# Kernel optimization log

Hardware: AMD Instinct MI355X
Metric: run time of the kernel (lower is better)

Reference implementation:

```python
import jax, jax.numpy as jnp
import numpy as np

N = 50000      # nodes per graph
E = 1_600_000  # edges per graph (before self-loops)
D = 128        # node feature dim
H = 9          # attention heads
C = 8          # channels per head
HC = H * C     # 72
NEG_SLOPE = 0.2


def setup_inputs() -> dict:
    key = jax.random.key(0)
    ks = iter(jax.random.split(key, 32))
    inp = {}
    for i in (1, 2, 3):
        inp[f"x{i}"] = jax.random.normal(next(ks), (N, D), dtype=jnp.float32)
        inp[f"edge_index{i}"] = jax.random.randint(next(ks), (2, E), 0, N, dtype=jnp.int64)
        inp[f"W{i}"] = jax.random.normal(next(ks), (D, HC), dtype=jnp.float32) * (1.0 / np.sqrt(D))
        inp[f"att_src{i}"] = jax.random.normal(next(ks), (H, C), dtype=jnp.float32) * 0.1
        inp[f"att_dst{i}"] = jax.random.normal(next(ks), (H, C), dtype=jnp.float32) * 0.1
        inp[f"b{i}"] = jnp.zeros((HC,), dtype=jnp.float32)
    inp["fnn_W"] = jax.random.normal(next(ks), (3 * HC, 2), dtype=jnp.float32) * (1.0 / np.sqrt(3 * HC))
    inp["fnn_b"] = jnp.zeros((2,), dtype=jnp.float32)
    return inp


def gat_conv(x, edge_index, W, att_src, att_dst, bias):
    """PyG GATConv (eval mode): linear -> per-edge LeakyReLU score -> edge softmax
    over incoming edges per dst node -> scatter-add aggregate. Self-loops added."""
    n = x.shape[0]
    loop = jnp.arange(n, dtype=edge_index.dtype)
    src = jnp.concatenate([edge_index[0], loop])  # [E+N]
    dst = jnp.concatenate([edge_index[1], loop])
    h = (x @ W).reshape(n, H, C)                  # [N,H,C]
    a_s = jnp.einsum('nhc,hc->nh', h, att_src)    # [N,H]
    a_d = jnp.einsum('nhc,hc->nh', h, att_dst)
    alpha = jax.nn.leaky_relu(a_s[src] + a_d[dst], NEG_SLOPE)   # [E+N,H]
    m = jax.ops.segment_max(alpha, dst, num_segments=n)         # stable softmax per dst
    alpha = jnp.exp(alpha - m[dst])
    denom = jax.ops.segment_sum(alpha, dst, num_segments=n)
    alpha = alpha / (denom[dst] + 1e-16)
    out = jax.ops.segment_sum(h[src] * alpha[:, :, None], dst, num_segments=n)
    return out.reshape(n, HC) + bias


def reference(x1, x2, x3, edge_index1, edge_index2, edge_index3,
              W1, att_src1, att_dst1, b1,
              W2, att_src2, att_dst2, b2,
              W3, att_src3, att_dst3, b3,
              fnn_W, fnn_b):
    o1 = gat_conv(x1, edge_index1, W1, att_src1, att_dst1, b1)
    o2 = gat_conv(x2, edge_index2, W2, att_src2, att_dst2, b2)
    o3 = gat_conv(x3, edge_index3, W3, att_src3, att_dst3, b3)
    x = jax.nn.relu(jnp.concatenate([o1, o2, o3], axis=1))  # [N, 216]
    logits = x @ fnn_W + fnn_b                              # [N, 2]
    return jax.nn.softmax(logits, axis=1)
```

## Files before the change

### kernel.cpp

```cpp
#include <hip/hip_runtime.h>
#include <hip/hip_fp16.h>

#define NN 50000
#define NE 1600000
#define DD 128
#define NH 9
#define NC 8
#define HCH 72
#define NEG 0.2f
#define NBUCK 196
#define NSEG 16
#define SPAD 17
#define EPB 16
#define BCH (256*EPB)
#define BSTRIDE 10240
#define BCSTRIDE 16
#define GEMMB2 ((NN + 63) / 64)
#define BINB ((NE + BCH - 1) / BCH)
#define AGGB ((NN * NH + 255) / 256)
#define CLP 88

typedef _Float16 f16x8 __attribute__((ext_vector_type(8)));
typedef float f32x4 __attribute__((ext_vector_type(4)));

__device__ __forceinline__ unsigned short f2h(float f) {
  return __half_as_ushort(__float2half_rn(f));
}
__device__ __forceinline__ float h2f(unsigned short u) {
  return __half2float(__ushort_as_half(u));
}
__device__ __forceinline__ float hlo(unsigned u) {
  return __half2float(__ushort_as_half((unsigned short)(u & 0xFFFFu)));
}
__device__ __forceinline__ float hhi(unsigned u) {
  return __half2float(__ushort_as_half((unsigned short)(u >> 16)));
}

struct GP {
  const float* x; const int* ei; const float* W;
  const float* as; const float* ad; const float* b;
  uint4* h2;
  unsigned short* as2;
  float* a_d; float* out;
  _Float16* wf;
  int* offs2;
  int* bcursor;
  unsigned int* pairs;
  int* csr;
};
struct GT { GP g[3]; };

__device__ __forceinline__ void accum(unsigned short u, uint4 v, float ad_n,
                                      float& denom, float4& acc0, float4& acc1) {
  float tt = h2f(u) + ad_n;
  tt = (tt > 0.f) ? tt : NEG * tt;
  const float w = __expf(tt);
  denom += w;
  acc0.x = fmaf(w, hlo(v.x), acc0.x); acc0.y = fmaf(w, hhi(v.x), acc0.y);
  acc0.z = fmaf(w, hlo(v.y), acc0.z); acc0.w = fmaf(w, hhi(v.y), acc0.w);
  acc1.x = fmaf(w, hlo(v.z), acc1.x); acc1.y = fmaf(w, hhi(v.z), acc1.y);
  acc1.z = fmaf(w, hlo(v.w), acc1.z); acc1.w = fmaf(w, hhi(v.w), acc1.w);
}

__global__ __launch_bounds__(256) void k_wpack(GT t) {
  const GP G = t.g[blockIdx.z];
  const int tid = threadIdx.x;
  for (int idx = tid; idx < 4 * 5 * 64 * 8; idx += 256) {
    const int j = idx & 7;
    const int lane = (idx >> 3) & 63;
    const int ctks = idx >> 9;
    const int ct = ctks % 5;
    const int ks = ctks / 5;
    const int k = ks * 32 + ((lane >> 4) << 3) + j;
    const int col = ct * 16 + (lane & 15);
    const float v = (col < HCH) ? G.W[k * HCH + col] : 0.f;
    G.wf[idx] = (_Float16)v;
  }
}

__global__ __launch_bounds__(256) void k_fat(GT t) {
  const GP G = t.g[blockIdx.z];
  __shared__ __align__(16) char smem[23072];
  const int tid = threadIdx.x;

  if (blockIdx.x < BINB) {
    unsigned* stage = (unsigned*)smem;
    unsigned char* bkt = (unsigned char*)(smem + 16384);
    int* hist   = (int*)(smem + 20480);
    int* gdelta = (int*)(smem + 21264);
    int* ssum   = (int*)(smem + 22048);
    const int e0 = blockIdx.x * BCH;

    for (int i = tid; i < NBUCK; i += 256) hist[i] = 0;
    __syncthreads();
    int dsts[EPB], srcs[EPB];
    #pragma unroll
    for (int k = 0; k < EPB; ++k) {
      const int e = e0 + k * 256 + tid;
      if (e < NE) {
        dsts[k] = G.ei[NE + e];
        srcs[k] = G.ei[e];
        atomicAdd(&hist[dsts[k] >> 8], 1);
      } else dsts[k] = -1;
    }
    __syncthreads();
    const int cnt_t = (tid < NBUCK) ? hist[tid] : 0;
    ssum[tid] = cnt_t;
    __syncthreads();
    int run = cnt_t;
    for (int off = 1; off < 256; off <<= 1) {
      int u = (tid >= off) ? ssum[tid - off] : 0;
      __syncthreads();
      run += u;
      ssum[tid] = run;
      __syncthreads();
    }
    const int excl = run - cnt_t;
    if (tid < NBUCK) {
      const int gbase = cnt_t ? atomicAdd(&G.bcursor[tid * BCSTRIDE], cnt_t) : 0;
      gdelta[tid] = tid * BSTRIDE + gbase - excl;
      hist[tid] = excl;
    }
    __syncthreads();
    #pragma unroll
    for (int k = 0; k < EPB; ++k) {
      if (dsts[k] >= 0) {
        const int b = dsts[k] >> 8;
        const int pos = atomicAdd(&hist[b], 1);
        stage[pos] = (unsigned)srcs[k] | ((unsigned)(dsts[k] & 255) << 16);
        bkt[pos] = (unsigned char)b;
      }
    }
    __syncthreads();
    const int total = (e0 + BCH <= NE) ? BCH : (NE - e0);
    for (int i = tid; i < total; i += 256) {
      const int b = bkt[i];
      const int addr = gdelta[b] + i;
      if (addr - b * BSTRIDE < BSTRIDE)
        G.pairs[addr] = stage[i];
    }
    return;
  }

  _Float16* Cl = (_Float16*)smem;
  const int wv = tid >> 6;
  const int ln = tid & 63;
  const int rl = ln & 15;
  const int kg = ln >> 4;
  const int n0 = (blockIdx.x - BINB) << 6;
  int arow = n0 + wv * 16 + rl;
  if (arow >= NN) arow = NN - 1;
  const float4* xr = (const float4*)(G.x + (size_t)arow * DD) + (kg << 1);
  const f16x8* wfp = (const f16x8*)G.wf;

  f32x4 acc[5];
  #pragma unroll
  for (int ct = 0; ct < 5; ++ct) acc[ct] = (f32x4){0.f, 0.f, 0.f, 0.f};

  #pragma unroll
  for (int ks = 0; ks < 4; ++ks) {
    const float4 xa = xr[ks * 8];
    const float4 xb = xr[ks * 8 + 1];
    float xs[8] = {xa.x, xa.y, xa.z, xa.w, xb.x, xb.y, xb.z, xb.w};
    f16x8 ahi, alo;
    #pragma unroll
    for (int j = 0; j < 8; ++j) {
      const _Float16 h = (_Float16)xs[j];
      ahi[j] = h;
      alo[j] = (_Float16)(xs[j] - (float)h);
    }
    #pragma unroll
    for (int ct = 0; ct < 5; ++ct) {
      const f16x8 bf = wfp[(ks * 5 + ct) * 64 + ln];
      acc[ct] = __builtin_amdgcn_mfma_f32_16x16x32_f16(ahi, bf, acc[ct], 0, 0, 0);
      acc[ct] = __builtin_amdgcn_mfma_f32_16x16x32_f16(alo, bf, acc[ct], 0, 0, 0);
    }
  }

  #pragma unroll
  for (int ct = 0; ct < 5; ++ct) {
    #pragma unroll
    for (int j = 0; j < 4; ++j)
      Cl[(wv * 16 + kg * 4 + j) * CLP + ct * 16 + rl] = (_Float16)acc[ct][j];
  }
  __syncthreads();

  for (int p = tid; p < 64 * NH; p += 256) {
    const int node = p / NH;
    const int hd = p - node * NH;
    const int n = n0 + node;
    if (n >= NN) continue;
    const uint4 hv = *(const uint4*)&Cl[node * CLP + hd * NC];
    const float h0 = hlo(hv.x), h1 = hhi(hv.x), h2v = hlo(hv.y), h3 = hhi(hv.y);
    const float h4 = hlo(hv.z), h5 = hhi(hv.z), h6 = hlo(hv.w), h7 = hhi(hv.w);
    const float4 As0 = *(const float4*)(G.as + hd * NC);
    const float4 As1 = *(const float4*)(G.as + hd * NC + 4);
    const float4 Ad0 = *(const float4*)(G.ad + hd * NC);
    const float4 Ad1 = *(const float4*)(G.ad + hd * NC + 4);
    const float ssrc = h0 * As0.x + h1 * As0.y + h2v * As0.z + h3 * As0.w
                     + h4 * As1.x + h5 * As1.y + h6 * As1.z + h7 * As1.w;
    const float sdst = h0 * Ad0.x + h1 * Ad0.y + h2v * Ad0.z + h3 * Ad0.w
                     + h4 * Ad1.x + h5 * Ad1.y + h6 * Ad1.z + h7 * Ad1.w;
    G.h2[(size_t)n * NH + hd] = hv;
    G.as2[n * NH + hd] = f2h(ssrc);
    G.a_d[n * NH + hd] = sdst;
  }
}

__global__ __launch_bounds__(256) void k_scat2(GT t) {
  const GP G = t.g[blockIdx.z];
  const int b = blockIdx.x;
  const int d0 = b << 8;
  __shared__ int cnt[256 * SPAD];
  __shared__ int ssum[256];
  __shared__ unsigned short stage[BSTRIDE];
  const int tid = threadIdx.x;
  const int estart = b * BSTRIDE;
  const int count0 = G.bcursor[b * BCSTRIDE];
  const int count = (count0 < BSTRIDE) ? count0 : BSTRIDE;
  const int eend = estart + count;
  for (int i = tid; i < 256 * SPAD; i += 256) cnt[i] = 0;
  __syncthreads();
  for (int e = estart + tid; e < eend; e += 256) {
    unsigned p = G.pairs[e];
    int key = (int)((p >> 16) * SPAD + ((p & 0xFFFFu) >> 12));
    atomicAdd(&cnt[key], 1);
  }
  __syncthreads();
  int local[NSEG];
  int sum = 0;
  #pragma unroll
  for (int i = 0; i < NSEG; ++i) { local[i] = sum; sum += cnt[tid * SPAD + i]; }
  ssum[tid] = sum;
  __syncthreads();
  int run = sum;
  for (int off = 1; off < 256; off <<= 1) {
    int u = (tid >= off) ? ssum[tid - off] : 0;
    __syncthreads();
    run += u;
    ssum[tid] = run;
    __syncthreads();
  }
  const int texcl = run - sum;
  int* o2 = G.offs2 + ((size_t)d0 << 4);
  #pragma unroll
  for (int i = 0; i < NSEG; ++i) {
    const int v = texcl + local[i];
    cnt[tid * SPAD + i] = v;
    o2[tid * NSEG + i] = estart + v;
  }
  __syncthreads();
  for (int e = estart + tid; e < eend; e += 256) {
    unsigned p = G.pairs[e];
    int key = (int)((p >> 16) * SPAD + ((p & 0xFFFFu) >> 12));
    int lpos = atomicAdd(&cnt[key], 1);
    if (lpos < BSTRIDE)
      stage[lpos] = (unsigned short)(p & 0xFFFFu);
  }
  __syncthreads();
  for (int i = tid; i < count; i += 256)
    G.csr[estart + i] = (int)stage[i];
}

__global__ __launch_bounds__(256) void k_agg(GT t) {
  const int g = blockIdx.x / AGGB;
  const GP G = t.g[g];
  const int gid = (blockIdx.x - g * AGGB) * 256 + threadIdx.x;
  const bool active = (gid < NN * NH);
  int n = 0, head = 0;
  if (active) { n = gid / NH; head = gid - n * NH; }
  float denom = 0.f;
  float4 acc0 = make_float4(0.f, 0.f, 0.f, 0.f);
  float4 acc1 = make_float4(0.f, 0.f, 0.f, 0.f);
  float ad_n = 0.f;
  int gb[5] = {0, 0, 0, 0, 0};
  if (active) {
    ad_n = G.a_d[n * NH + head];
    const int* o2 = G.offs2 + ((size_t)n << 4);
    gb[0] = o2[0]; gb[1] = o2[4]; gb[2] = o2[8]; gb[3] = o2[12]; gb[4] = o2[13];
    float sl = h2f(G.as2[n * NH + head]) + ad_n;
    sl = (sl > 0.f) ? sl : NEG * sl;
    float wl = __expf(sl);
    uint4 hs = G.h2[(size_t)n * NH + head];
    denom = wl;
    acc0.x = wl * hlo(hs.x); acc0.y = wl * hhi(hs.x);
    acc0.z = wl * hlo(hs.y); acc0.w = wl * hhi(hs.y);
    acc1.x = wl * hlo(hs.z); acc1.y = wl * hhi(hs.z);
    acc1.z = wl * hlo(hs.w); acc1.w = wl * hhi(hs.w);
  }
  #pragma unroll
  for (int sgrp = 0; sgrp < 4; ++sgrp) {
    int e = gb[sgrp];
    const int en = gb[sgrp + 1];
    for (; e + 8 <= en; e += 8) {
      const int s0 = G.csr[e];
      const int s1 = G.csr[e + 1];
      const int s2 = G.csr[e + 2];
      const int s3 = G.csr[e + 3];
      const int s4 = G.csr[e + 4];
      const int s5 = G.csr[e + 5];
      const int s6 = G.csr[e + 6];
      const int s7 = G.csr[e + 7];
      const unsigned short u0 = G.as2[s0 * NH + head];
      const unsigned short u1 = G.as2[s1 * NH + head];
      const unsigned short u2 = G.as2[s2 * NH + head];
      const unsigned short u3 = G.as2[s3 * NH + head];
      const unsigned short u4 = G.as2[s4 * NH + head];
      const unsigned short u5 = G.as2[s5 * NH + head];
      const unsigned short u6 = G.as2[s6 * NH + head];
      const unsigned short u7 = G.as2[s7 * NH + head];
      const uint4 v0 = G.h2[(size_t)s0 * NH + head];
      const uint4 v1 = G.h2[(size_t)s1 * NH + head];
      const uint4 v2 = G.h2[(size_t)s2 * NH + head];
      const uint4 v3 = G.h2[(size_t)s3 * NH + head];
      const uint4 v4 = G.h2[(size_t)s4 * NH + head];
      const uint4 v5 = G.h2[(size_t)s5 * NH + head];
      const uint4 v6 = G.h2[(size_t)s6 * NH + head];
      const uint4 v7 = G.h2[(size_t)s7 * NH + head];
      accum(u0, v0, ad_n, denom, acc0, acc1);
      accum(u1, v1, ad_n, denom, acc0, acc1);
      accum(u2, v2, ad_n, denom, acc0, acc1);
      accum(u3, v3, ad_n, denom, acc0, acc1);
      accum(u4, v4, ad_n, denom, acc0, acc1);
      accum(u5, v5, ad_n, denom, acc0, acc1);
      accum(u6, v6, ad_n, denom, acc0, acc1);
      accum(u7, v7, ad_n, denom, acc0, acc1);
    }
    if (e + 4 <= en) {
      const int s0 = G.csr[e];
      const int s1 = G.csr[e + 1];
      const int s2 = G.csr[e + 2];
      const int s3 = G.csr[e + 3];
      const unsigned short u0 = G.as2[s0 * NH + head];
      const unsigned short u1 = G.as2[s1 * NH + head];
      const unsigned short u2 = G.as2[s2 * NH + head];
      const unsigned short u3 = G.as2[s3 * NH + head];
      const uint4 v0 = G.h2[(size_t)s0 * NH + head];
      const uint4 v1 = G.h2[(size_t)s1 * NH + head];
      const uint4 v2 = G.h2[(size_t)s2 * NH + head];
      const uint4 v3 = G.h2[(size_t)s3 * NH + head];
      accum(u0, v0, ad_n, denom, acc0, acc1);
      accum(u1, v1, ad_n, denom, acc0, acc1);
      accum(u2, v2, ad_n, denom, acc0, acc1);
      accum(u3, v3, ad_n, denom, acc0, acc1);
      e += 4;
    }
    for (; e < en; ++e) {
      const int src = G.csr[e];
      const unsigned short u = G.as2[src * NH + head];
      const uint4 hv = G.h2[(size_t)src * NH + head];
      accum(u, hv, ad_n, denom, acc0, acc1);
    }
    __builtin_amdgcn_s_barrier();
  }
  if (!active) return;
  float inv = 1.f / (denom + 1e-16f);
  const float* bp = G.b + head * NC;
  float4 o0, o1;
  o0.x = acc0.x * inv + bp[0]; o0.y = acc0.y * inv + bp[1];
  o0.z = acc0.z * inv + bp[2]; o0.w = acc0.w * inv + bp[3];
  o1.x = acc1.x * inv + bp[4]; o1.y = acc1.y * inv + bp[5];
  o1.z = acc1.z * inv + bp[6]; o1.w = acc1.w * inv + bp[7];
  float4* op = (float4*)(G.out + (size_t)n * HCH + head * NC);
  op[0] = o0; op[1] = o1;
}

__global__ __launch_bounds__(256) void k_fnn(const float* __restrict__ o1,
                                             const float* __restrict__ o2,
                                             const float* __restrict__ o3,
                                             const float* __restrict__ fw,
                                             const float* __restrict__ fb,
                                             float* __restrict__ out) {
  const int tid = blockIdx.x * 256 + threadIdx.x;
  const int n = tid >> 6;
  const int lane = tid & 63;
  if (n >= NN) return;
  float acc0 = 0.f, acc1 = 0.f;
  for (int j = lane; j < 3 * HCH; j += 64) {
    const int g = j / HCH;
    const int c = j - g * HCH;
    const float* og = (g == 0) ? o1 : (g == 1) ? o2 : o3;
    float v = og[(size_t)n * HCH + c];
    v = v > 0.f ? v : 0.f;
    acc0 = fmaf(v, fw[2 * j], acc0);
    acc1 = fmaf(v, fw[2 * j + 1], acc1);
  }
  #pragma unroll
  for (int off = 32; off > 0; off >>= 1) {
    acc0 += __shfl_down(acc0, off, 64);
    acc1 += __shfl_down(acc1, off, 64);
  }
  if (lane == 0) {
    float l0 = acc0 + fb[0], l1 = acc1 + fb[1];
    float m = fmaxf(l0, l1);
    float e0 = __expf(l0 - m), e1 = __expf(l1 - m);
    float inv = 1.f / (e0 + e1);
    out[(size_t)n * 2] = e0 * inv;
    out[(size_t)n * 2 + 1] = e1 * inv;
  }
}

extern "C" void kernel_launch(void* const* d_in, const int* in_sizes, int n_in,
                              void* d_out, int out_size, void* d_ws, size_t ws_size,
                              hipStream_t stream) {
  (void)in_sizes; (void)n_in; (void)out_size; (void)ws_size;
  GT t;
  char* w = (char*)d_ws;
  size_t off = 0;
  auto carve = [&](size_t bytes) -> void* {
    void* p = w + off;
    off = (off + bytes + 255) & ~(size_t)255;
    return p;
  };
  int* bc_all = (int*)carve(3 * NBUCK * BCSTRIDE * 4);
  for (int g = 0; g < 3; ++g) {
    GP& G = t.g[g];
    G.x  = (const float*)d_in[6 * g + 0];
    G.ei = (const int*)d_in[6 * g + 1];
    G.W  = (const float*)d_in[6 * g + 2];
    G.as = (const float*)d_in[6 * g + 3];
    G.ad = (const float*)d_in[6 * g + 4];
    G.b  = (const float*)d_in[6 * g + 5];
    G.bcursor = bc_all + g * NBUCK * BCSTRIDE;
    G.h2   = (uint4*)carve((size_t)NN * NH * 16);
    G.as2  = (unsigned short*)carve((size_t)NN * NH * 2);
    G.a_d  = (float*)carve((size_t)NN * NH * 4);
    G.out  = (float*)carve((size_t)NN * HCH * 4);
    G.wf   = (_Float16*)carve((size_t)4 * 5 * 64 * 8 * 2);
    G.offs2 = (int*)carve((size_t)NBUCK * 256 * NSEG * 4);
    G.pairs = (unsigned int*)carve((size_t)NBUCK * BSTRIDE * 4);
    G.csr   = (int*)carve((size_t)NBUCK * BSTRIDE * 4);
  }
  const float* fw = (const float*)d_in[18];
  const float* fb = (const float*)d_in[19];
  float* outp = (float*)d_out;

  dim3 b256(256, 1, 1);
  hipMemsetAsync(bc_all, 0, 3 * NBUCK * BCSTRIDE * 4, stream);
  k_wpack <<<dim3(1, 1, 3), b256, 0, stream>>>(t);
  k_fat   <<<dim3(BINB + GEMMB2, 1, 3), b256, 0, stream>>>(t);
  k_scat2 <<<dim3(NBUCK, 1, 3), b256, 0, stream>>>(t);
  k_agg   <<<dim3(AGGB * 3, 1, 1), b256, 0, stream>>>(t);
  k_fnn   <<<(NN * 64 + 255) / 256, b256, 0, stream>>>(t.g[0].out, t.g[1].out, t.g[2].out, fw, fb, outp);
}
```

Measured before the change: 406.4 us.

## Recompute source attention score from gathered features instead of loading as2

Drops the precomputed fp16 per-node source score array. The aggregation kernel now recomputes the dot product of the gathered h row with att_src for each edge, which removes one scattered 2-byte gather per edge at the cost of 8 extra FMAs. The bucket-cursor memset is folded into the weight-pack kernel, saving a separate memset launch. The edge loop unroll drops from 8 to 4 and the per-group barrier becomes __syncthreads. Risks include more ALU work per edge and less memory-level parallelism from the smaller unroll.

Result: faster. 386.1 us (-5.0%).

```diff
diff --git a/kernel.cpp b/kernel.cpp
--- a/kernel.cpp
+++ b/kernel.cpp
@@ -40,7 +40,6 @@
   const float* x; const int* ei; const float* W;
   const float* as; const float* ad; const float* b;
   uint4* h2;
-  unsigned short* as2;
   float* a_d; float* out;
   _Float16* wf;
   int* offs2;
@@ -50,21 +49,27 @@
 };
 struct GT { GP g[3]; };
 
-__device__ __forceinline__ void accum(unsigned short u, uint4 v, float ad_n,
-                                      float& denom, float4& acc0, float4& acc1) {
-  float tt = h2f(u) + ad_n;
+__device__ __forceinline__ void accum2(uint4 v, const float4 As0, const float4 As1,
+                                       float ad_n, float& denom,
+                                       float4& acc0, float4& acc1) {
+  const float h0 = hlo(v.x), h1 = hhi(v.x), h2v = hlo(v.y), h3 = hhi(v.y);
+  const float h4 = hlo(v.z), h5 = hhi(v.z), h6 = hlo(v.w), h7 = hhi(v.w);
+  const float s = h0 * As0.x + h1 * As0.y + h2v * As0.z + h3 * As0.w
+                + h4 * As1.x + h5 * As1.y + h6 * As1.z + h7 * As1.w;
+  float tt = s + ad_n;
   tt = (tt > 0.f) ? tt : NEG * tt;
   const float w = __expf(tt);
   denom += w;
-  acc0.x = fmaf(w, hlo(v.x), acc0.x); acc0.y = fmaf(w, hhi(v.x), acc0.y);
-  acc0.z = fmaf(w, hlo(v.y), acc0.z); acc0.w = fmaf(w, hhi(v.y), acc0.w);
-  acc1.x = fmaf(w, hlo(v.z), acc1.x); acc1.y = fmaf(w, hhi(v.z), acc1.y);
-  acc1.z = fmaf(w, hlo(v.w), acc1.z); acc1.w = fmaf(w, hhi(v.w), acc1.w);
+  acc0.x = fmaf(w, h0, acc0.x); acc0.y = fmaf(w, h1, acc0.y);
+  acc0.z = fmaf(w, h2v, acc0.z); acc0.w = fmaf(w, h3, acc0.w);
+  acc1.x = fmaf(w, h4, acc1.x); acc1.y = fmaf(w, h5, acc1.y);
+  acc1.z = fmaf(w, h6, acc1.z); acc1.w = fmaf(w, h7, acc1.w);
 }
 
 __global__ __launch_bounds__(256) void k_wpack(GT t) {
   const GP G = t.g[blockIdx.z];
   const int tid = threadIdx.x;
+  for (int i = tid; i < NBUCK * BCSTRIDE; i += 256) G.bcursor[i] = 0;
   for (int idx = tid; idx < 4 * 5 * 64 * 8; idx += 256) {
     const int j = idx & 7;
     const int lane = (idx >> 3) & 63;
@@ -193,16 +198,11 @@
     const uint4 hv = *(const uint4*)&Cl[node * CLP + hd * NC];
     const float h0 = hlo(hv.x), h1 = hhi(hv.x), h2v = hlo(hv.y), h3 = hhi(hv.y);
     const float h4 = hlo(hv.z), h5 = hhi(hv.z), h6 = hlo(hv.w), h7 = hhi(hv.w);
-    const float4 As0 = *(const float4*)(G.as + hd * NC);
-    const float4 As1 = *(const float4*)(G.as + hd * NC + 4);
     const float4 Ad0 = *(const float4*)(G.ad + hd * NC);
     const float4 Ad1 = *(const float4*)(G.ad + hd * NC + 4);
-    const float ssrc = h0 * As0.x + h1 * As0.y + h2v * As0.z + h3 * As0.w
-                     + h4 * As1.x + h5 * As1.y + h6 * As1.z + h7 * As1.w;
     const float sdst = h0 * Ad0.x + h1 * Ad0.y + h2v * Ad0.z + h3 * Ad0.w
                      + h4 * Ad1.x + h5 * Ad1.y + h6 * Ad1.z + h7 * Ad1.w;
     G.h2[(size_t)n * NH + hd] = hv;
-    G.as2[n * NH + hd] = f2h(ssrc);
     G.a_d[n * NH + hd] = sdst;
   }
 }
@@ -273,85 +273,42 @@
   float4 acc0 = make_float4(0.f, 0.f, 0.f, 0.f);
   float4 acc1 = make_float4(0.f, 0.f, 0.f, 0.f);
   float ad_n = 0.f;
+  float4 As0 = make_float4(0.f, 0.f, 0.f, 0.f);
+  float4 As1 = make_float4(0.f, 0.f, 0.f, 0.f);
   int gb[5] = {0, 0, 0, 0, 0};
   if (active) {
     ad_n = G.a_d[n * NH + head];
+    As0 = *(const float4*)(G.as + head * NC);
+    As1 = *(const float4*)(G.as + head * NC + 4);
     const int* o2 = G.offs2 + ((size_t)n << 4);
     gb[0] = o2[0]; gb[1] = o2[4]; gb[2] = o2[8]; gb[3] = o2[12]; gb[4] = o2[13];
-    float sl = h2f(G.as2[n * NH + head]) + ad_n;
-    sl = (sl > 0.f) ? sl : NEG * sl;
-    float wl = __expf(sl);
-    uint4 hs = G.h2[(size_t)n * NH + head];
-    denom = wl;
-    acc0.x = wl * hlo(hs.x); acc0.y = wl * hhi(hs.x);
-    acc0.z = wl * hlo(hs.y); acc0.w = wl * hhi(hs.y);
-    acc1.x = wl * hlo(hs.z); acc1.y = wl * hhi(hs.z);
-    acc1.z = wl * hlo(hs.w); acc1.w = wl * hhi(hs.w);
+    const uint4 hs = G.h2[(size_t)n * NH + head];
+    accum2(hs, As0, As1, ad_n, denom, acc0, acc1);
   }
   #pragma unroll
   for (int sgrp = 0; sgrp < 4; ++sgrp) {
     int e = gb[sgrp];
     const int en = gb[sgrp + 1];
-    for (; e + 8 <= en; e += 8) {
+    for (; e + 4 <= en; e += 4) {
       const int s0 = G.csr[e];
       const int s1 = G.csr[e + 1];
       const int s2 = G.csr[e + 2];
       const int s3 = G.csr[e + 3];
-      const int s4 = G.csr[e + 4];
-      const int s5 = G.csr[e + 5];
-      const int s6 = G.csr[e + 6];
-      const int s7 = G.csr[e + 7];
-      const unsigned short u0 = G.as2[s0 * NH + head];
-      const unsigned short u1 = G.as2[s1 * NH + head];
-      const unsigned short u2 = G.as2[s2 * NH + head];
-      const unsigned short u3 = G.as2[s3 * NH + head];
-      const unsigned short u4 = G.as2[s4 * NH + head];
-      const unsigned short u5 = G.as2[s5 * NH + head];
-      const unsigned short u6 = G.as2[s6 * NH + head];
-      const unsigned short u7 = G.as2[s7 * NH + head];
       const uint4 v0 = G.h2[(size_t)s0 * NH + head];
       const uint4 v1 = G.h2[(size_t)s1 * NH + head];
       const uint4 v2 = G.h2[(size_t)s2 * NH + head];
       const uint4 v3 = G.h2[(size_t)s3 * NH + head];
-      const uint4 v4 = G.h2[(size_t)s4 * NH + head];
-      const uint4 v5 = G.h2[(size_t)s5 * NH + head];
-      const uint4 v6 = G.h2[(size_t)s6 * NH + head];
-      const uint4 v7 = G.h2[(size_t)s7 * NH + head];
-      accum(u0, v0, ad_n, denom, acc0, acc1);
-      accum(u1, v1, ad_n, denom, acc0, acc1);
-      accum(u2, v2, ad_n, denom, acc0, acc1);
-      accum(u3, v3, ad_n, denom, acc0, acc1);
-      accum(u4, v4, ad_n, denom, acc0, acc1);
-      accum(u5, v5, ad_n, denom, acc0, acc1);
-      accum(u6, v6, ad_n, denom, acc0, acc1);
-      accum(u7, v7, ad_n, denom, acc0, acc1);
-    }
-    if (e + 4 <= en) {
-      const int s0 = G.csr[e];
-      const int s1 = G.csr[e + 1];
-      const int s2 = G.csr[e + 2];
-      const int s3 = G.csr[e + 3];
-      const unsigned short u0 = G.as2[s0 * NH + head];
-      const unsigned short u1 = G.as2[s1 * NH + head];
-      const unsigned short u2 = G.as2[s2 * NH + head];
-      const unsigned short u3 = G.as2[s3 * NH + head];
-      const uint4 v0 = G.h2[(size_t)s0 * NH + head];
-      const uint4 v1 = G.h2[(size_t)s1 * NH + head];
-      const uint4 v2 = G.h2[(size_t)s2 * NH + head];
-      const uint4 v3 = G.h2[(size_t)s3 * NH + head];
-      accum(u0, v0, ad_n, denom, acc0, acc1);
-      accum(u1, v1, ad_n, denom, acc0, acc1);
-      accum(u2, v2, ad_n, denom, acc0, acc1);
-      accum(u3, v3, ad_n, denom, acc0, acc1);
-      e += 4;
+      accum2(v0, As0, As1, ad_n, denom, acc0, acc1);
+      accum2(v1, As0, As1, ad_n, denom, acc0, acc1);
+      accum2(v2, As0, As1, ad_n, denom, acc0, acc1);
+      accum2(v3, As0, As1, ad_n, denom, acc0, acc1);
     }
     for (; e < en; ++e) {
       const int src = G.csr[e];
-      const unsigned short u = G.as2[src * NH + head];
       const uint4 hv = G.h2[(size_t)src * NH + head];
-      accum(u, hv, ad_n, denom, acc0, acc1);
-    }
-    __builtin_amdgcn_s_barrier();
+      accum2(hv, As0, As1, ad_n, denom, acc0, acc1);
+    }
+    __syncthreads();
   }
   if (!active) return;
   float inv = 1.f / (denom + 1e-16f);
@@ -423,7 +380,6 @@
     G.b  = (const float*)d_in[6 * g + 5];
     G.bcursor = bc_all + g * NBUCK * BCSTRIDE;
     G.h2   = (uint4*)carve((size_t)NN * NH * 16);
-    G.as2  = (unsigned short*)carve((size_t)NN * NH * 2);
     G.a_d  = (float*)carve((size_t)NN * NH * 4);
     G.out  = (float*)carve((size_t)NN * HCH * 4);
     G.wf   = (_Float16*)carve((size_t)4 * 5 * 64 * 8 * 2);
@@ -436,7 +392,6 @@
   float* outp = (float*)d_out;
 
   dim3 b256(256, 1, 1);
-  hipMemsetAsync(bc_all, 0, 3 * NBUCK * BCSTRIDE * 4, stream);
   k_wpack <<<dim3(1, 1, 3), b256, 0, stream>>>(t);
   k_fat   <<<dim3(BINB + GEMMB2, 1, 3), b256, 0, stream>>>(t);
   k_scat2 <<<dim3(NBUCK, 1, 3), b256, 0, stream>>>(t);
```
